# Optimization experiments

Hardware: AMD Instinct MI355X
Metric: run time of the kernel (lower is better)

The kernel has to match this reference:

```python
import jax, jax.numpy as jnp
import numpy as np

S = 3072        # total packed tokens
E = 1280        # d_model
H = 20          # encoder_attention_heads
D = E // H      # head_dim = 64
NSEG = 16       # number of packed audio chunks


def setup_inputs() -> dict:
    key = jax.random.key(0)
    ks = jax.random.split(key, 9)
    w = lambda k, shape: (jax.random.normal(k, shape, jnp.float32) * 0.02)
    hidden_states = jax.random.normal(ks[0], (S, E), jnp.float32)
    cu_seqlens = (jnp.arange(NSEG + 1, dtype=jnp.int32) * (S // NSEG))
    return {
        "hidden_states": hidden_states,
        "Wq": w(ks[1], (E, E)), "bq": w(ks[2], (E,)),
        "Wk": w(ks[3], (E, E)),                      # k_proj has no bias
        "Wv": w(ks[4], (E, E)), "bv": w(ks[5], (E,)),
        "Wo": w(ks[6], (E, E)), "bo": w(ks[7], (E,)),
        "cu_seqlens": cu_seqlens,
    }


def reference(hidden_states, Wq, bq, Wk, Wv, bv, Wo, bo, cu_seqlens):
    Sq, Em = hidden_states.shape
    Dh = Em // H
    # projections (torch Linear: x @ W.T + b)
    q = (hidden_states @ Wq.T + bq).reshape(Sq, H, Dh).transpose(1, 0, 2)  # [H,S,D]
    k = (hidden_states @ Wk.T).reshape(Sq, H, Dh).transpose(1, 0, 2)       # [H,S,D]
    v = (hidden_states @ Wv.T + bv).reshape(Sq, H, Dh).transpose(1, 0, 2)  # [H,S,D]
    # block-diagonal additive mask from cu_seqlens (vectorized equivalent of
    # the original Python loop): tokens attend only within their own segment.
    pos = jnp.arange(Sq)
    seg = jnp.searchsorted(cu_seqlens[1:], pos, side="right")              # segment id per token
    same = seg[:, None] == seg[None, :]                                    # [S,S]
    bias = jnp.where(same, 0.0, jnp.finfo(q.dtype).min)
    attn = jnp.einsum("hqd,hkd->hqk", q, k) / np.sqrt(Dh).astype(q.dtype)  # [H,S,S]
    attn = jax.nn.softmax(attn + bias, axis=-1)
    out = jnp.einsum("hqk,hkd->hqd", attn, v)                              # [H,S,D]
    out = out.transpose(1, 0, 2).reshape(Sq, Em)
    return out @ Wo.T + bo
```

## Files before the change

kernel.cpp:

```cpp
#include <hip/hip_runtime.h>
#include <hip/hip_bf16.h>
#include <stdint.h>

#define S_TOK 3072
#define E_DIM 1280
#define H_NUM 20
#define D_HEAD 64
#define NSEG 16

typedef __attribute__((ext_vector_type(8))) short short8;
typedef __attribute__((ext_vector_type(4))) float f32x4;

__device__ __forceinline__ unsigned short f2bf(float f){
  union { float f; unsigned int i; } u; u.f = f;
  unsigned int r = u.i + 0x7FFFu + ((u.i >> 16) & 1u);
  return (unsigned short)(r >> 16);
}

__device__ __forceinline__ void gload_lds16(const void* g, void* l){
  __builtin_amdgcn_global_load_lds((__attribute__((address_space(1))) void*)(g),
                                   (__attribute__((address_space(3))) void*)(l), 16, 0, 0);
}

__global__ void cvt_all(const float* __restrict__ hs,
                        const float* __restrict__ w0, const float* __restrict__ w1,
                        const float* __restrict__ w2,
                        unsigned short* __restrict__ hsb,
                        unsigned short* __restrict__ dqkv,
                        int nHS4, int nW4){
  int i = blockIdx.x * blockDim.x + threadIdx.x;
  const float* src;
  unsigned short* dst;
  size_t sj, dj;
  if (i < nHS4){
    src = hs; dst = hsb; sj = i; dj = i;
  } else {
    int t = i - nHS4;
    int w = t / nW4;
    if (w >= 3) return;
    int j = t - w * nW4;
    src = (w == 0) ? w0 : (w == 1) ? w1 : w2;
    sj = j;
    dst = dqkv; dj = (size_t)w * nW4 + j;
  }
  float4 v = reinterpret_cast<const float4*>(src)[sj];
  ushort4 o;
  o.x = f2bf(v.x); o.y = f2bf(v.y); o.z = f2bf(v.z); o.w = f2bf(v.w);
  reinterpret_cast<ushort4*>(dst)[dj] = o;
}

template<int MODE>
__global__ __launch_bounds__(MODE==0?512:256, 2) void gemm_ph(
    const unsigned short* __restrict__ A,
    const unsigned short* __restrict__ Bp,
    const float* __restrict__ bias0,
    const float* __restrict__ bias1,
    unsigned short* __restrict__ Oq,
    unsigned short* __restrict__ Ok,
    unsigned short* __restrict__ Ov,
    float* __restrict__ Of,
    int M, int N, int K)
{
  constexpr int BM    = MODE==0 ? 256 : 128;
  constexpr int BLOCK = MODE==0 ? 512 : 256;
  constexpr int HR    = BM/2;
  constexpr int HS    = HR*64;
  constexpr int MR2   = MODE==0 ? 4 : 2;

  __shared__ __align__(16) unsigned short SH[8*HS];

  const int nwg = gridDim.x;
  const int xcd = blockIdx.x & 7, ix = blockIdx.x >> 3;
  const int qq = nwg >> 3, rr8 = nwg & 7;
  const int wg = (xcd < rr8 ? xcd*(qq+1) : rr8*(qq+1) + (xcd-rr8)*qq) + ix;
  const int nbn = N / BM;
  const int sgn = nbn / 5;
  const int st = wg / 20, ii = wg % 20;
  const int bm = (st / sgn) * 4 + ii / 5;
  const int bn = (st % sgn) * 5 + ii % 5;
  const int row0 = bm * BM, col0 = bn * BM;

  const int tid  = threadIdx.x;
  const int lane = tid & 63;
  const int w    = tid >> 6;
  const int wm   = MODE==0 ? (w >> 2) : (w >> 1);
  const int wn   = MODE==0 ? (w & 3) : (w & 1);

  const f32x4 fz = {0.f, 0.f, 0.f, 0.f};
  f32x4 acc[4][MR2][2];
#pragma unroll
  for (int qd = 0; qd < 4; ++qd)
#pragma unroll
    for (int m = 0; m < MR2; ++m)
#pragma unroll
      for (int n = 0; n < 2; ++n) acc[qd][m][n] = fz;

  const int s1 = tid, s2 = BLOCK + tid;
  const int r1 = s1 >> 3, ks1 = (s1 & 7) ^ (r1 & 7);
  const int r2 = s2 >> 3, ks2 = (s2 & 7) ^ (r2 & 7);

  auto stA = [&](int h, int t){
    unsigned short* d = SH + ((t & 1) * 4 + h) * HS;
    const unsigned short* g = A + (size_t)(row0 + h*HR) * K + (t << 6);
    gload_lds16(g + (size_t)r1*K + ks1*8, d + s1*8);
    gload_lds16(g + (size_t)r2*K + ks2*8, d + s2*8);
  };
  auto stB = [&](int h, int t){
    unsigned short* d = SH + ((t & 1) * 4 + 2 + h) * HS;
    const unsigned short* g = Bp + (size_t)(col0 + h*HR) * K + (t << 6);
    gload_lds16(g + (size_t)r1*K + ks1*8, d + s1*8);
    gload_lds16(g + (size_t)r2*K + ks2*8, d + s2*8);
  };

  short8 af[MR2][2], bf0[2][2], bf1[2][2];
  auto RA = [&](int mh, int db){
    const unsigned short* Ah = SH + (db*4 + mh)*HS;
#pragma unroll
    for (int m = 0; m < MR2; ++m){
      int ra = wm*(HR/2) + m*16 + (lane & 15);
#pragma unroll
      for (int kk = 0; kk < 2; ++kk){
        int sl = kk*4 + (lane >> 4);
        af[m][kk] = *reinterpret_cast<const short8*>(&Ah[ra*64 + ((sl ^ (ra & 7)))*8]);
      }
    }
  };
  auto RB = [&](int nh, int db, short8 (*bf)[2]){
    const unsigned short* Bh = SH + (db*4 + 2 + nh)*HS;
#pragma unroll
    for (int n = 0; n < 2; ++n){
      int rb = wn*32 + n*16 + (lane & 15);
#pragma unroll
      for (int kk = 0; kk < 2; ++kk){
        int sl = kk*4 + (lane >> 4);
        bf[n][kk] = *reinterpret_cast<const short8*>(&Bh[rb*64 + ((sl ^ (rb & 7)))*8]);
      }
    }
  };

#define MF_Q(QD, BF)                                                          \
  do {                                                                        \
    __builtin_amdgcn_s_setprio(1);                                            \
    _Pragma("unroll")                                                         \
    for (int kk = 0; kk < 2; ++kk)                                            \
      _Pragma("unroll")                                                       \
      for (int m = 0; m < MR2; ++m)                                           \
        _Pragma("unroll")                                                     \
        for (int n = 0; n < 2; ++n)                                           \
          acc[QD][m][n] = __builtin_amdgcn_mfma_f32_16x16x32_bf16(            \
              af[m][kk], BF[n][kk], acc[QD][m][n], 0, 0, 0);                  \
    __builtin_amdgcn_s_setprio(0);                                            \
  } while (0)

  const int nk = K >> 6;
  stA(0,0); stB(0,0); stB(1,0); stA(1,0);

  for (int t = 0; t < nk; ++t){
    const int db = t & 1;
    const bool nx = (t + 1 < nk);
    asm volatile("s_waitcnt vmcnt(4)" ::: "memory");
    __builtin_amdgcn_s_barrier();
    RA(0, db); RB(0, db, bf0);
    if (nx) stA(0, t+1);
    asm volatile("s_waitcnt lgkmcnt(0)" ::: "memory");
    __builtin_amdgcn_sched_barrier(0);
    MF_Q(0, bf0);
    if (nx) asm volatile("s_waitcnt vmcnt(4)" ::: "memory");
    else    asm volatile("s_waitcnt vmcnt(2)" ::: "memory");
    __builtin_amdgcn_s_barrier();
    RB(1, db, bf1);
    if (nx) stB(0, t+1);
    asm volatile("s_waitcnt lgkmcnt(0)" ::: "memory");
    __builtin_amdgcn_sched_barrier(0);
    MF_Q(1, bf1);
    if (nx) asm volatile("s_waitcnt vmcnt(4)" ::: "memory");
    else    asm volatile("s_waitcnt vmcnt(0)" ::: "memory");
    __builtin_amdgcn_s_barrier();
    RA(1, db);
    if (nx) stB(1, t+1);
    asm volatile("s_waitcnt lgkmcnt(0)" ::: "memory");
    __builtin_amdgcn_sched_barrier(0);
    MF_Q(2, bf1);
    __builtin_amdgcn_s_barrier();
    if (nx) stA(1, t+1);
    MF_Q(3, bf0);
  }
  __syncthreads();

  if (MODE == 0){
    unsigned short* Cs = SH;
    const int CSTR = 264;
    const int mat = col0 / E_DIM;
    const int cc0 = col0 - mat * E_DIM;
    unsigned short* dst = (mat == 0) ? Oq : ((mat == 1) ? Ok : Ov);
    float bb[2][2];
#pragma unroll
    for (int nh = 0; nh < 2; ++nh)
#pragma unroll
      for (int n = 0; n < 2; ++n){
        int cc = cc0 + nh*128 + wn*32 + n*16 + (lane & 15);
        bb[nh][n] = (mat == 0) ? bias0[cc] : (mat == 2 ? bias1[cc] : 0.0f);
      }
#pragma unroll
    for (int ph = 0; ph < 2; ++ph){
#pragma unroll
      for (int q2i = 0; q2i < 2; ++q2i){
        const int qd = ph*2 + q2i;
        const int nh = (qd >> 1) ^ (qd & 1);
#pragma unroll
        for (int m = 0; m < MR2; ++m)
#pragma unroll
          for (int n = 0; n < 2; ++n)
#pragma unroll
            for (int j = 0; j < 4; ++j){
              int rr = wm*64 + m*16 + (lane >> 4)*4 + j;
              int c  = nh*128 + wn*32 + n*16 + (lane & 15);
              Cs[rr * CSTR + c] = f2bf(acc[qd][m][n][j] + bb[nh][n]);
            }
      }
      __syncthreads();
#pragma unroll
      for (int i = 0; i < 8; ++i){
        int tk  = i * 512 + tid;
        int p   = tk >> 10;
        int idx = tk & 1023;
        int rr  = idx >> 3, sq = idx & 7;
        short8 vv = *reinterpret_cast<const short8*>(&Cs[rr * CSTR + p * 64 + sq * 8]);
        int gr = row0 + ph * 128 + rr;
        int hh = (cc0 >> 6) + p;
        *reinterpret_cast<short8*>(&dst[((size_t)hh * S_TOK + gr) * D_HEAD + sq * 8]) = vv;
      }
      __syncthreads();
    }
  } else {
    float bc[2][2];
#pragma unroll
    for (int nh = 0; nh < 2; ++nh)
#pragma unroll
      for (int n = 0; n < 2; ++n)
        bc[nh][n] = bias0[col0 + nh*64 + wn*32 + n*16 + (lane & 15)];
#pragma unroll
    for (int qd = 0; qd < 4; ++qd){
      const int mh = qd >> 1;
      const int nh = (qd >> 1) ^ (qd & 1);
#pragma unroll
      for (int m = 0; m < MR2; ++m)
#pragma unroll
        for (int n = 0; n < 2; ++n){
          int c = col0 + nh*64 + wn*32 + n*16 + (lane & 15);
#pragma unroll
          for (int j = 0; j < 4; ++j){
            int r = row0 + mh*64 + wm*32 + m*16 + (lane >> 4)*4 + j;
            Of[(size_t)r * E_DIM + c] = acc[qd][m][n][j] + bc[nh][n];
          }
        }
    }
  }
#undef MF_Q
}

#define VSTR 200
#define PSTR 72
#define ATTN_BLKS (H_NUM * NSEG * 3)
__global__ __launch_bounds__(256, 3) void attn_kernel(
    const unsigned short* __restrict__ Q,
    const unsigned short* __restrict__ Kb,
    const unsigned short* __restrict__ V,
    const int* __restrict__ cu,
    unsigned short* __restrict__ O,
    const float* __restrict__ Wo,
    unsigned short* __restrict__ wob,
    int nW4)
{
  __shared__ __align__(16) unsigned short Vt[64*VSTR];
  __shared__ __align__(16) unsigned short Pw[4][16][PSTR];

  const int bid  = blockIdx.x;
  if (bid >= ATTN_BLKS){
    int i = (bid - ATTN_BLKS) * 256 + threadIdx.x;
    if (i < nW4){
      float4 v = reinterpret_cast<const float4*>(Wo)[i];
      ushort4 o;
      o.x = f2bf(v.x); o.y = f2bf(v.y); o.z = f2bf(v.z); o.w = f2bf(v.w);
      reinterpret_cast<ushort4*>(wob)[i] = o;
    }
    return;
  }
  const int unit = bid / 3;
  const int third= bid - unit*3;
  const int h    = unit >> 4;
  const int seg  = unit & 15;
  const int s0   = cu[seg];
  const int L    = cu[seg + 1] - s0;
  if (L <= 0) return;

  const int tid  = threadIdx.x;
  const int lane = tid & 63;
  const int w    = tid >> 6;
  const int row0g = third*64 + w*16;

  const unsigned short* qh = Q  + (size_t)h * S_TOK * D_HEAD;
  const unsigned short* kh = Kb + (size_t)h * S_TOK * D_HEAD;
  const unsigned short* vh = V  + (size_t)h * S_TOK * D_HEAD;

#pragma unroll
  for (int i = 0; i < 6; ++i){
    int task = i*256 + tid;
    int sr   = task % 192;
    int grp  = task / 192;
    int svr  = s0 + (sr < L ? sr : L - 1);
    short8 vv = *reinterpret_cast<const short8*>(vh + (size_t)svr*64 + grp*8);
#pragma unroll
    for (int j = 0; j < 8; ++j) Vt[(grp*8 + j)*VSTR + sr] = (unsigned short)vv[j];
  }

  short8 qf[2];
#pragma unroll
  for (int kk = 0; kk < 2; ++kk){
    int r  = row0g + (lane & 15);
    int sr = s0 + (r < L ? r : L - 1);
    qf[kk] = *reinterpret_cast<const short8*>(qh + (size_t)sr*64 + kk*32 + (lane >> 4)*8);
  }

  __syncthreads();

  const f32x4 fz = {0.f, 0.f, 0.f, 0.f};
  const float SCL = 0.125f * 1.44269504088896f;

  f32x4 sacc[12];
#pragma unroll
  for (int nt = 0; nt < 12; ++nt) sacc[nt] = fz;

#pragma unroll
  for (int nt = 0; nt < 12; ++nt){
    int rb = nt*16 + (lane & 15);
    int sr = s0 + (rb < L ? rb : L - 1);
    const unsigned short* kr = kh + (size_t)sr*64 + (lane >> 4)*8;
    short8 kf0 = *reinterpret_cast<const short8*>(kr);
    short8 kf1 = *reinterpret_cast<const short8*>(kr + 32);
    sacc[nt] = __builtin_amdgcn_mfma_f32_16x16x32_bf16(qf[0], kf0, sacc[nt], 0, 0, 0);
    sacc[nt] = __builtin_amdgcn_mfma_f32_16x16x32_bf16(qf[1], kf1, sacc[nt], 0, 0, 0);
  }

  float rinv[4];
#pragma unroll
  for (int j = 0; j < 4; ++j){
    float mx = -1e30f;
#pragma unroll
    for (int nt = 0; nt < 12; ++nt){
      int c = nt*16 + (lane & 15);
      float vv = (c < L) ? sacc[nt][j] : -1e30f;
      sacc[nt][j] = vv;
      mx = fmaxf(mx, vv);
    }
    mx = fmaxf(mx, __shfl_xor(mx, 1, 64));
    mx = fmaxf(mx, __shfl_xor(mx, 2, 64));
    mx = fmaxf(mx, __shfl_xor(mx, 4, 64));
    mx = fmaxf(mx, __shfl_xor(mx, 8, 64));
    float sum = 0.f;
#pragma unroll
    for (int nt = 0; nt < 12; ++nt){
      float pp = exp2f((sacc[nt][j] - mx) * SCL);
      sacc[nt][j] = pp;
      sum += pp;
    }
    sum += __shfl_xor(sum, 1, 64);
    sum += __shfl_xor(sum, 2, 64);
    sum += __shfl_xor(sum, 4, 64);
    sum += __shfl_xor(sum, 8, 64);
    rinv[j] = 1.0f / sum;
  }

  f32x4 oacc[4];
#pragma unroll
  for (int nt = 0; nt < 4; ++nt) oacc[nt] = fz;

#pragma unroll
  for (int kk = 0; kk < 6; ++kk){
#pragma unroll
    for (int ntl = 0; ntl < 2; ++ntl){
      int nt = kk*2 + ntl;
#pragma unroll
      for (int j = 0; j < 4; ++j)
        Pw[w][(lane >> 4)*4 + j][ntl*16 + (lane & 15)] = f2bf(sacc[nt][j]);
    }
    short8 pf = *reinterpret_cast<const short8*>(&Pw[w][lane & 15][(lane >> 4)*8]);
#pragma unroll
    for (int nt4 = 0; nt4 < 4; ++nt4){
      int dcol = nt4*16 + (lane & 15);
      short8 vf = *reinterpret_cast<const short8*>(&Vt[dcol*VSTR + kk*32 + (lane >> 4)*8]);
      oacc[nt4] = __builtin_amdgcn_mfma_f32_16x16x32_bf16(pf, vf, oacc[nt4], 0, 0, 0);
    }
  }

#pragma unroll
  for (int nt4 = 0; nt4 < 4; ++nt4)
#pragma unroll
    for (int j = 0; j < 4; ++j)
      Pw[w][(lane >> 4)*4 + j][nt4*16 + (lane & 15)] = f2bf(oacc[nt4][j] * rinv[j]);

  {
    int r = lane >> 2;
    int gr = row0g + r;
    if (gr < L){
#pragma unroll
      for (int part = 0; part < 2; ++part){
        int c0 = (lane & 3)*16 + part*8;
        short8 vv = *reinterpret_cast<const short8*>(&Pw[w][r][c0]);
        *reinterpret_cast<short8*>(&O[(size_t)(s0 + gr) * E_DIM + h*64 + c0]) = vv;
      }
    }
  }
}

extern "C" void kernel_launch(void* const* d_in, const int* in_sizes, int n_in,
                              void* d_out, int out_size, void* d_ws, size_t ws_size,
                              hipStream_t stream)
{
  const float* hs = (const float*)d_in[0];
  const float* Wq = (const float*)d_in[1];
  const float* bq = (const float*)d_in[2];
  const float* Wk = (const float*)d_in[3];
  const float* Wv = (const float*)d_in[4];
  const float* bv = (const float*)d_in[5];
  const float* Wo = (const float*)d_in[6];
  const float* bo = (const float*)d_in[7];
  const int*   cu = (const int*)d_in[8];
  float* out = (float*)d_out;

  unsigned short* p = (unsigned short*)d_ws;
  unsigned short* hsb  = p; p += (size_t)S_TOK * E_DIM;
  unsigned short* wqkv = p; p += (size_t)3 * E_DIM * E_DIM;
  unsigned short* wob  = p; p += (size_t)E_DIM * E_DIM;
  unsigned short* qb   = p; p += (size_t)S_TOK * E_DIM;
  unsigned short* kb   = p; p += (size_t)S_TOK * E_DIM;
  unsigned short* vb   = p; p += (size_t)S_TOK * E_DIM;
  unsigned short* aob  = p; p += (size_t)S_TOK * E_DIM;

  const int nHS4 = S_TOK * E_DIM / 4;
  const int nW4  = E_DIM * E_DIM / 4;
  const int nCvt = nHS4 + 3 * nW4;
  cvt_all<<<(nCvt + 255) / 256, 256, 0, stream>>>(hs, Wq, Wk, Wv, hsb, wqkv, nHS4, nW4);

  gemm_ph<0><<<(S_TOK/256) * (3*E_DIM/256), 512, 0, stream>>>(
      hsb, wqkv, bq, bv, qb, kb, vb, nullptr, S_TOK, 3*E_DIM, E_DIM);

  const int cvtWoBlks = (nW4 + 255) / 256;
  attn_kernel<<<ATTN_BLKS + cvtWoBlks, 256, 0, stream>>>(
      qb, kb, vb, cu, aob, Wo, wob, nW4);

  gemm_ph<1><<<(S_TOK/128) * (E_DIM/128), 256, 0, stream>>>(
      aob, wob, bo, nullptr, nullptr, nullptr, nullptr, out, S_TOK, E_DIM, E_DIM);
}
```

Baseline: 93.76 us.

## Deepen GEMM K-loop prefetch to two stages ahead with peeled tail

Restructures the GEMM main loop so global-to-LDS loads for tile t+2 are issued while tile t is computed, instead of just one tile ahead. A prologue preloads the second tile and an epilogue iteration handles the last tile with tighter vmcnt waits. The aim is to hide more global memory latency behind MFMA work. In exchange it adds extra barriers per quarter-step, and the buffer reuse ordering is more fragile.

Result: no change. 95.49 us (+1.8%).

```diff
diff --git a/kernel.cpp b/kernel.cpp
--- a/kernel.cpp
+++ b/kernel.cpp
@@ -50,7 +50,7 @@
 }
 
 template<int MODE>
-__global__ __launch_bounds__(MODE==0?512:256, 2) void gemm_ph(
+__global__ __launch_bounds__(MODE==0?512:256, MODE==0?2:2) void gemm_ph(
     const unsigned short* __restrict__ A,
     const unsigned short* __restrict__ Bp,
     const float* __restrict__ bias0,
@@ -152,37 +152,46 @@
     __builtin_amdgcn_s_setprio(0);                                            \
   } while (0)
 
+#define LGKM0 do { asm volatile("s_waitcnt lgkmcnt(0)" ::: "memory");         \
+                   __builtin_amdgcn_sched_barrier(0); } while (0)
+#define BAR   __builtin_amdgcn_s_barrier()
+
   const int nk = K >> 6;
   stA(0,0); stB(0,0); stB(1,0); stA(1,0);
-
-  for (int t = 0; t < nk; ++t){
+  stA(0,1); stB(0,1); stB(1,1);
+  asm volatile("s_waitcnt vmcnt(6)" ::: "memory");
+  BAR;
+
+  for (int t = 0; t < nk - 1; ++t){
     const int db = t & 1;
-    const bool nx = (t + 1 < nk);
-    asm volatile("s_waitcnt vmcnt(4)" ::: "memory");
-    __builtin_amdgcn_s_barrier();
+    const bool f2 = (t + 2 < nk);
     RA(0, db); RB(0, db, bf0);
-    if (nx) stA(0, t+1);
-    asm volatile("s_waitcnt lgkmcnt(0)" ::: "memory");
-    __builtin_amdgcn_sched_barrier(0);
-    MF_Q(0, bf0);
-    if (nx) asm volatile("s_waitcnt vmcnt(4)" ::: "memory");
-    else    asm volatile("s_waitcnt vmcnt(2)" ::: "memory");
-    __builtin_amdgcn_s_barrier();
+    stA(1, t+1);
+    BAR; LGKM0; MF_Q(0, bf0); BAR;
     RB(1, db, bf1);
-    if (nx) stB(0, t+1);
-    asm volatile("s_waitcnt lgkmcnt(0)" ::: "memory");
-    __builtin_amdgcn_sched_barrier(0);
-    MF_Q(1, bf1);
-    if (nx) asm volatile("s_waitcnt vmcnt(4)" ::: "memory");
-    else    asm volatile("s_waitcnt vmcnt(0)" ::: "memory");
-    __builtin_amdgcn_s_barrier();
+    if (f2) stA(0, t+2);
+    BAR; LGKM0; MF_Q(1, bf1); BAR;
     RA(1, db);
-    if (nx) stB(1, t+1);
-    asm volatile("s_waitcnt lgkmcnt(0)" ::: "memory");
-    __builtin_amdgcn_sched_barrier(0);
-    MF_Q(2, bf1);
-    __builtin_amdgcn_s_barrier();
-    if (nx) stA(1, t+1);
+    if (f2) stB(0, t+2);
+    BAR; LGKM0; MF_Q(2, bf1); BAR;
+    if (f2) stB(1, t+2);
+    BAR; MF_Q(3, bf0);
+    if (f2) asm volatile("s_waitcnt vmcnt(6)" ::: "memory");
+    else    asm volatile("s_waitcnt vmcnt(4)" ::: "memory");
+    BAR;
+  }
+  {
+    const int db = (nk - 1) & 1;
+    RA(0, db); RB(0, db, bf0);
+    BAR; LGKM0; MF_Q(0, bf0);
+    asm volatile("s_waitcnt vmcnt(2)" ::: "memory");
+    BAR;
+    RB(1, db, bf1);
+    BAR; LGKM0; MF_Q(1, bf1);
+    asm volatile("s_waitcnt vmcnt(0)" ::: "memory");
+    BAR;
+    RA(1, db);
+    BAR; LGKM0; MF_Q(2, bf1); BAR;
     MF_Q(3, bf0);
   }
   __syncthreads();
@@ -257,6 +266,8 @@
     }
   }
 #undef MF_Q
+#undef LGKM0
+#undef BAR
 }
 
 #define VSTR 200
```
